# Optimization experiments

Measured on AMD Instinct MI355X. Metric: run time of the kernel, lower is better.

## Reference

```python
import jax, jax.numpy as jnp
import numpy as np

N_HEADS = 32
N_KV_HEADS = 8
HEAD_DIM = 128
ROPE_BASE = 10000.0
NEG_INF = -1e9


def rope(x, base=ROPE_BASE, offset=0):
    # x: [B, H, L, d]; 'traditional' RoPE with the module's rotation formula.
    d = x.shape[-1]
    t = jnp.arange(x.shape[2], dtype=jnp.float32) + offset
    freqs = base ** (-jnp.arange(0, d, 2, dtype=jnp.float32) / d)  # [d/2]
    ang = t[:, None] * freqs[None, :]                              # [L, d/2]
    cos, sin = jnp.cos(ang), jnp.sin(ang)
    x1, x2 = x[..., 0::2], x[..., 1::2]
    out = jnp.stack([x1 * cos + x2 * sin, x1 * sin - x2 * cos], axis=-1)
    return out.reshape(x.shape)


def setup_inputs() -> dict:
    key = jax.random.key(0)
    ks = jax.random.split(key, 5)
    B, L, D = 2, 2048, 4096
    x = jax.random.normal(ks[0], (B, L, D), dtype=jnp.float32)
    wq = jax.random.normal(ks[1], (D, N_HEADS * HEAD_DIM), dtype=jnp.float32) * 0.02
    wk = jax.random.normal(ks[2], (D, N_KV_HEADS * HEAD_DIM), dtype=jnp.float32) * 0.02
    wv = jax.random.normal(ks[3], (D, N_KV_HEADS * HEAD_DIM), dtype=jnp.float32) * 0.02
    wo = jax.random.normal(ks[4], (N_HEADS * HEAD_DIM, D), dtype=jnp.float32) * 0.02
    # causal additive mask [L, L]
    mask = jnp.where(jnp.tril(jnp.ones((L, L), dtype=bool)), 0.0, NEG_INF).astype(jnp.float32)
    return {"x": x, "mask": mask, "wq": wq, "wk": wk, "wv": wv, "wo": wo}


def reference(x, mask, wq, wk, wv, wo):
    B, L, D = x.shape
    scale = HEAD_DIM ** -0.5
    q = (x @ wq).reshape(B, L, N_HEADS, HEAD_DIM).transpose(0, 2, 1, 3)     # [B,H,L,d]
    k = (x @ wk).reshape(B, L, N_KV_HEADS, HEAD_DIM).transpose(0, 2, 1, 3)  # [B,Hk,L,d]
    v = (x @ wv).reshape(B, L, N_KV_HEADS, HEAD_DIM).transpose(0, 2, 1, 3)
    rep = N_HEADS // N_KV_HEADS
    k = jnp.repeat(k, rep, axis=1)  # [B,H,L,d]  (physical GQA repeat, as in source)
    v = jnp.repeat(v, rep, axis=1)
    q = rope(q)
    k = rope(k)
    scores = jnp.einsum("bhqd,bhkd->bhqk", q * scale, k) + mask  # [B,H,L,L]
    probs = jax.nn.softmax(scores.astype(jnp.float32), axis=-1).astype(scores.dtype)
    out = jnp.einsum("bhqk,bhkd->bhqd", probs, v)
    out = out.transpose(0, 2, 1, 3).reshape(B, L, N_HEADS * HEAD_DIM)
    return out @ wo, (k, v)
```

## Files before the change

kernel.cpp:

```cpp
#include <hip/hip_runtime.h>

typedef unsigned short u16;
typedef unsigned int u32;
typedef float f32x4 __attribute__((ext_vector_type(4)));
typedef u32 u32x2 __attribute__((ext_vector_type(2)));
typedef __bf16 bf16x8 __attribute__((ext_vector_type(8)));

#define DEV __device__ __forceinline__

DEV u16 f2b(float f) {
    union { float f; u32 u; } v; v.f = f;
    u32 r = v.u + 0x7fffu + ((v.u >> 16) & 1u);
    return (u16)(r >> 16);
}
DEV float b2f(u16 b) {
    union { u32 u; float f; } v; v.u = ((u32)b) << 16;
    return v.f;
}

DEV void gload16(const void* g, void* l) {
    __builtin_amdgcn_global_load_lds((const __attribute__((address_space(1))) void*)g,
                                     (__attribute__((address_space(3))) void*)l, 16, 0, 0);
}

DEV f32x4 mfma16(bf16x8 a, bf16x8 b, f32x4 c) {
    return __builtin_amdgcn_mfma_f32_16x16x32_bf16(a, b, c, 0, 0, 0);
}

__global__ __launch_bounds__(256) void convx_kernel(const float* __restrict__ in,
                                                    u16* __restrict__ out) {
    size_t i = ((size_t)blockIdx.x * 256 + threadIdx.x) * 4;
    float4 v = *(const float4*)(in + i);
    ushort4 o; o.x = f2b(v.x); o.y = f2b(v.y); o.z = f2b(v.z); o.w = f2b(v.w);
    *(ushort4*)(out + i) = o;
}

__global__ __launch_bounds__(256) void tconv_kernel(const float* __restrict__ in,
                                                    u16* __restrict__ out, int K, int N) {
    __shared__ float tile[64][65];
    int t = threadIdx.x;
    int n0 = blockIdx.x * 64, k0 = blockIdx.y * 64;
    int r = t >> 4, c4 = (t & 15) * 4;
#pragma unroll
    for (int i = 0; i < 4; ++i) {
        float4 v = *(const float4*)(in + (size_t)(k0 + i * 16 + r) * N + n0 + c4);
        tile[i * 16 + r][c4 + 0] = v.x; tile[i * 16 + r][c4 + 1] = v.y;
        tile[i * 16 + r][c4 + 2] = v.z; tile[i * 16 + r][c4 + 3] = v.w;
    }
    __syncthreads();
#pragma unroll
    for (int i = 0; i < 4; ++i) {
        int nn = i * 16 + r;
        ushort4 o;
        o.x = f2b(tile[c4 + 0][nn]); o.y = f2b(tile[c4 + 1][nn]);
        o.z = f2b(tile[c4 + 2][nn]); o.w = f2b(tile[c4 + 3][nn]);
        *(ushort4*)(out + (size_t)(n0 + nn) * K + k0 + c4) = o;
    }
}

#define GEMM128_BODY                                                                        \
    __shared__ __align__(16) u16 Asb[2][2][64 * 64];                                        \
    __shared__ __align__(16) u16 Bsb[2][2][64 * 64];                                        \
    int t = threadIdx.x;                                                                    \
    int lane = t & 63, w = t >> 6;                                                          \
    int wrM = w >> 1, wcN = w & 1;                                                          \
    int lr = lane & 15, hi = lane >> 4;                                                     \
    int wg = blockIdx.x;                                                                    \
    int swz = (wg & 7) * ((int)gridDim.x >> 3) + (wg >> 3);                                 \
    int bx = swz / gy, by = swz % gy;                                                       \
    int m0 = by * 128, n0 = bx * 128;                                                       \
    int nk = K >> 6;                                                                        \
    auto stageA = [&](int X, int h) {                                                       \
        const u16* src = A + (size_t)(m0 + h * 64) * K + X * 64;                            \
        char* dst = (char*)&Asb[X & 1][h][0];                                               \
        _Pragma("unroll")                                                                   \
        for (int it = 0; it < 2; ++it) {                                                    \
            int c = it * 256 + t;                                                           \
            int row = c >> 3;                                                               \
            int col8 = ((c & 7) ^ (row & 7)) << 3;                                          \
            gload16(src + (size_t)row * K + col8, dst + (it * 256 + (t & ~63)) * 16);       \
        }                                                                                   \
    };                                                                                      \
    auto stageB = [&](int X, int h) {                                                       \
        const u16* src = Bt + (size_t)(n0 + h * 64) * K + X * 64;                           \
        char* dst = (char*)&Bsb[X & 1][h][0];                                               \
        _Pragma("unroll")                                                                   \
        for (int it = 0; it < 2; ++it) {                                                    \
            int c = it * 256 + t;                                                           \
            int row = c >> 3;                                                               \
            int col8 = ((c & 7) ^ (row & 7)) << 3;                                          \
            gload16(src + (size_t)row * K + col8, dst + (it * 256 + (t & ~63)) * 16);       \
        }                                                                                   \
    };                                                                                      \
    stageA(0, 0); stageA(0, 1); stageB(0, 0); stageB(0, 1);                                 \
    stageA(1, 0); stageA(1, 1);                                                             \
    asm volatile("s_waitcnt vmcnt(4)" ::: "memory");                                        \
    __builtin_amdgcn_s_barrier();                                                           \
    f32x4 acc[4][4] = {};                                                                   \
    for (int kt = 0; kt < nk; ++kt) {                                                       \
        __builtin_amdgcn_sched_barrier(0);                                                  \
        int p = kt & 1;                                                                     \
        const char* Ah = (const char*)&Asb[p][wrM][0];                                      \
        const char* Bh = (const char*)&Bsb[p][wcN][0];                                      \
        bool s1 = (kt + 1 < nk), s2 = (kt + 2 < nk);                                        \
        bf16x8 a[4][2], bb[2][2];                                                           \
        _Pragma("unroll")                                                                   \
        for (int mf = 0; mf < 4; ++mf)                                                      \
            _Pragma("unroll")                                                               \
            for (int ks = 0; ks < 2; ++ks) {                                                \
                int row = mf * 16 + lr;                                                     \
                a[mf][ks] = *(const bf16x8*)(Ah + ((row * 128 + ks * 64 + hi * 16) ^ ((row & 7) << 4))); \
            }                                                                               \
        _Pragma("unroll")                                                                   \
        for (int nf = 0; nf < 2; ++nf)                                                      \
            _Pragma("unroll")                                                               \
            for (int ks = 0; ks < 2; ++ks) {                                                \
                int row = nf * 16 + lr;                                                     \
                bb[nf][ks] = *(const bf16x8*)(Bh + ((row * 128 + ks * 64 + hi * 16) ^ ((row & 7) << 4))); \
            }                                                                               \
        if (s1) { stageB(kt + 1, 0); stageB(kt + 1, 1); }                                   \
        __builtin_amdgcn_s_barrier();                                                       \
        __builtin_amdgcn_s_setprio(1);                                                      \
        _Pragma("unroll")                                                                   \
        for (int mf = 0; mf < 4; ++mf)                                                      \
            _Pragma("unroll")                                                               \
            for (int nf = 0; nf < 2; ++nf)                                                  \
                _Pragma("unroll")                                                           \
                for (int ks = 0; ks < 2; ++ks)                                              \
                    acc[mf][nf] = mfma16(a[mf][ks], bb[nf][ks], acc[mf][nf]);               \
        __builtin_amdgcn_s_setprio(0);                                                      \
        __builtin_amdgcn_s_barrier();                                                       \
        _Pragma("unroll")                                                                   \
        for (int nf = 0; nf < 2; ++nf)                                                      \
            _Pragma("unroll")                                                               \
            for (int ks = 0; ks < 2; ++ks) {                                                \
                int row = (nf + 2) * 16 + lr;                                               \
                bb[nf][ks] = *(const bf16x8*)(Bh + ((row * 128 + ks * 64 + hi * 16) ^ ((row & 7) << 4))); \
            }                                                                               \
        if (s2) { stageA(kt + 2, 0); stageA(kt + 2, 1); }                                   \
        __builtin_amdgcn_s_barrier();                                                       \
        __builtin_amdgcn_s_setprio(1);                                                      \
        _Pragma("unroll")                                                                   \
        for (int mf = 0; mf < 4; ++mf)                                                      \
            _Pragma("unroll")                                                               \
            for (int nf = 0; nf < 2; ++nf)                                                  \
                _Pragma("unroll")                                                           \
                for (int ks = 0; ks < 2; ++ks)                                              \
                    acc[mf][nf + 2] = mfma16(a[mf][ks], bb[nf][ks], acc[mf][nf + 2]);       \
        __builtin_amdgcn_s_setprio(0);                                                      \
        if (s2)      asm volatile("s_waitcnt vmcnt(4)" ::: "memory");                       \
        else if (s1) asm volatile("s_waitcnt vmcnt(0)" ::: "memory");                       \
        __builtin_amdgcn_s_barrier();                                                       \
    }

__global__ __launch_bounds__(256, 2) void gemm128_qkv_kernel(const u16* __restrict__ A,
                                                             const u16* __restrict__ Bt,
                                                             u16* __restrict__ Cb,
                                                             float* __restrict__ outk,
                                                             int N, int K, int gy) {
    GEMM128_BODY
    int isv = (n0 >= 5120);
    int isk = (n0 >= 4096) && !isv;
    int odd = lane & 1;
#pragma unroll
    for (int nf = 0; nf < 4; ++nf) {
        int n = n0 + wcN * 64 + nf * 16 + lr;
        int d = n & 127;
        float freq = exp2f((float)(d >> 1) * -0.2076205059304601f);
#pragma unroll
        for (int mf = 0; mf < 4; ++mf)
#pragma unroll
            for (int r = 0; r < 4; ++r) {
                int m = m0 + wrM * 64 + mf * 16 + hi * 4 + r;
                int l = m & 2047, bi = m >> 11;
                float val = acc[mf][nf][r];
                float pair = __shfl_xor(val, 1);
                float out = val;
                if (!isv) {
                    float sv, cv;
                    sincosf((float)l * freq, &sv, &cv);
                    out = odd ? (pair * sv - val * cv) : (val * cv + pair * sv);
                }
                Cb[(size_t)m * N + n] = f2b(out);
                if (isk) {
                    int kvh = (n - 4096) >> 7;
#pragma unroll
                    for (int rr = 0; rr < 4; ++rr)
                        outk[((size_t)((bi * 32 + kvh * 4 + rr) * 2048) + l) * 128 + d] = out;
                }
            }
    }
}

__global__ __launch_bounds__(256, 2) void gemm128_kernel(const u16* __restrict__ A,
                                                         const u16* __restrict__ Bt,
                                                         float* __restrict__ Cf,
                                                         int N, int K, int gy) {
    GEMM128_BODY
#pragma unroll
    for (int mf = 0; mf < 4; ++mf)
#pragma unroll
        for (int nf = 0; nf < 4; ++nf)
#pragma unroll
            for (int r = 0; r < 4; ++r) {
                int m = m0 + wrM * 64 + mf * 16 + hi * 4 + r;
                int n = n0 + wcN * 64 + nf * 16 + lr;
                Cf[(size_t)m * N + n] = acc[mf][nf][r];
            }
}

__global__ __launch_bounds__(256) void vtrans_kernel(const u16* __restrict__ qkv,
                                                     u16* __restrict__ vt,
                                                     float* __restrict__ outv) {
    __shared__ u16 tile[64][65];
    int t = threadIdx.x;
    int l0 = blockIdx.x * 64, d0 = blockIdx.y * 64;
    int z = blockIdx.z, b = z >> 3, kvh = z & 7;
    int r = t >> 4, c4 = (t & 15) * 4;
#pragma unroll
    for (int i = 0; i < 4; ++i) {
        int l = l0 + i * 16 + r;
        ushort4 v = *(const ushort4*)(qkv + (size_t)(b * 2048 + l) * 6144 + 5120 + kvh * 128 + d0 + c4);
        tile[i * 16 + r][c4 + 0] = v.x; tile[i * 16 + r][c4 + 1] = v.y;
        tile[i * 16 + r][c4 + 2] = v.z; tile[i * 16 + r][c4 + 3] = v.w;
        float4 f; f.x = b2f(v.x); f.y = b2f(v.y); f.z = b2f(v.z); f.w = b2f(v.w);
#pragma unroll
        for (int rr = 0; rr < 4; ++rr)
            *(float4*)(outv + ((size_t)((b * 32 + kvh * 4 + rr) * 2048) + l) * 128 + d0 + c4) = f;
    }
    __syncthreads();
#pragma unroll
    for (int i = 0; i < 4; ++i) {
        int dn = i * 16 + r;
        ushort4 o;
        o.x = tile[c4 + 0][dn]; o.y = tile[c4 + 1][dn];
        o.z = tile[c4 + 2][dn]; o.w = tile[c4 + 3][dn];
        *(ushort4*)(vt + (size_t)((b * 8 + kvh) * 128 + d0 + dn) * 2048 + l0 + c4) = o;
    }
}

__global__ __launch_bounds__(256, 2) void attn_kernel(const u16* __restrict__ qkv,
                                                      const u16* __restrict__ vt,
                                                      u16* __restrict__ ab) {
    __shared__ __align__(16) u16 Kbuf[2][64 * 128];
    __shared__ __align__(16) u16 Vbuf[2][128 * 64];
    __shared__ __align__(16) u16 Ps[4][32 * 64];
    int t = threadIdx.x, lane = t & 63, w = t >> 6;
    int lr = lane & 15, hi = lane >> 4;
    int h = blockIdx.y, b = blockIdx.z, kvh = h >> 2;

    const u16* kbase = qkv + (size_t)(b * 2048) * 6144 + 4096 + kvh * 128;
    const u16* vtbase = vt + (size_t)((b * 8 + kvh) * 128) * 2048;

    auto stageKV = [&](int k0, int buf) {
#pragma unroll
        for (int i = 0; i < 4; ++i) {
            int c = i * 256 + t;
            int row = c >> 4;
            int col8 = ((c & 15) ^ (row & 7)) << 3;
            gload16(kbase + (size_t)(k0 + row) * 6144 + col8,
                    (char*)Kbuf[buf] + (i * 256 + (t & ~63)) * 16);
        }
#pragma unroll
        for (int i = 0; i < 4; ++i) {
            int c = i * 256 + t;
            int row = c >> 3;
            int col8 = ((c & 7) ^ (row & 7)) << 3;
            gload16(vtbase + (size_t)row * 2048 + k0 + col8,
                    (char*)Vbuf[buf] + (i * 256 + (t & ~63)) * 16);
        }
    };

    auto process = [&](int qblk) {
        int q0 = qblk * 128;
        bf16x8 qf[2][4];
#pragma unroll
        for (int half = 0; half < 2; ++half)
#pragma unroll
            for (int kki = 0; kki < 4; ++kki)
                qf[half][kki] = *(const bf16x8*)(qkv +
                    (size_t)(b * 2048 + q0 + w * 32 + half * 16 + lr) * 6144 + h * 128 +
                    kki * 32 + 8 * hi);
        f32x4 acc[2][8] = {};
        float mrun[2] = {-1e30f, -1e30f}, lrun[2] = {0.f, 0.f};

        int nt = 2 * (qblk + 1);
        stageKV(0, 0);
        __syncthreads();
        int cur = 0;
        for (int kt = 0; kt < nt; ++kt) {
            if (kt + 1 < nt) stageKV((kt + 1) * 64, cur ^ 1);
            __builtin_amdgcn_sched_barrier(0);

            const u16* Ks = Kbuf[cur];
            const u16* Vs = Vbuf[cur];
            f32x4 s[2][4] = {};
            __builtin_amdgcn_s_setprio(1);
#pragma unroll
            for (int kki = 0; kki < 4; ++kki) {
                bf16x8 kf[4];
#pragma unroll
                for (int fc = 0; fc < 4; ++fc) {
                    int kvr = fc * 16 + lr;
                    int byt = (kvr * 256 + (kki * 32 + 8 * hi) * 2) ^ ((kvr & 7) << 4);
                    kf[fc] = *(const bf16x8*)((const char*)Ks + byt);
                }
#pragma unroll
                for (int fc = 0; fc < 4; ++fc) {
                    s[0][fc] = mfma16(kf[fc], qf[0][kki], s[0][fc]);
                    s[1][fc] = mfma16(kf[fc], qf[1][kki], s[1][fc]);
                }
            }
            __builtin_amdgcn_s_setprio(0);
            const float SC = 0.08838834764831845f;
            int domask = (kt >= nt - 2);
            u16* Pw = Ps[w];
#pragma unroll
            for (int half = 0; half < 2; ++half) {
                int qabs = q0 + w * 32 + half * 16 + lr;
#pragma unroll
                for (int fc = 0; fc < 4; ++fc)
#pragma unroll
                    for (int r = 0; r < 4; ++r) {
                        float v = s[half][fc][r] * SC;
                        if (domask && (kt * 64 + fc * 16 + hi * 4 + r) > qabs) v = -1e30f;
                        s[half][fc][r] = v;
                    }
                float pm = s[half][0][0];
#pragma unroll
                for (int fc = 0; fc < 4; ++fc)
#pragma unroll
                    for (int r = 0; r < 4; ++r) pm = fmaxf(pm, s[half][fc][r]);
                pm = fmaxf(pm, __shfl_xor(pm, 16));
                pm = fmaxf(pm, __shfl_xor(pm, 32));
                float mn = fmaxf(mrun[half], pm);
                float fr = __expf(mrun[half] - mn);
                mrun[half] = mn;
                float ls = 0.f;
#pragma unroll
                for (int fc = 0; fc < 4; ++fc)
#pragma unroll
                    for (int r = 0; r < 4; ++r) {
                        float e = __expf(s[half][fc][r] - mn);
                        s[half][fc][r] = e;
                        ls += e;
                    }
                ls += __shfl_xor(ls, 16);
                ls += __shfl_xor(ls, 32);
                lrun[half] = lrun[half] * fr + ls;
#pragma unroll
                for (int dhf = 0; dhf < 8; ++dhf)
#pragma unroll
                    for (int r = 0; r < 4; ++r) acc[half][dhf][r] *= fr;
#pragma unroll
                for (int fc = 0; fc < 4; ++fc) {
                    u32x2 pk;
                    pk.x = (u32)f2b(s[half][fc][0]) | ((u32)f2b(s[half][fc][1]) << 16);
                    pk.y = (u32)f2b(s[half][fc][2]) | ((u32)f2b(s[half][fc][3]) << 16);
                    int byt = (half * 2048 + lr * 128 + fc * 32 + hi * 8) ^ ((lr & 7) << 4);
                    *(u32x2*)((char*)Pw + byt) = pk;
                }
            }
            asm volatile("s_waitcnt lgkmcnt(0)" ::: "memory");
            __builtin_amdgcn_s_setprio(1);
#pragma unroll
            for (int kk2 = 0; kk2 < 2; ++kk2) {
                bf16x8 pf0 = *(const bf16x8*)((const char*)Pw +
                    ((lr * 128 + kk2 * 64 + hi * 16) ^ ((lr & 7) << 4)));
                bf16x8 pf1 = *(const bf16x8*)((const char*)Pw +
                    ((2048 + lr * 128 + kk2 * 64 + hi * 16) ^ ((lr & 7) << 4)));
#pragma unroll
                for (int dhf = 0; dhf < 8; ++dhf) {
                    int dh = dhf * 16 + lr;
                    int bytv = (dh * 128 + (kk2 * 32 + 8 * hi) * 2) ^ ((dh & 7) << 4);
                    bf16x8 vf = *(const bf16x8*)((const char*)Vs + bytv);
                    acc[0][dhf] = mfma16(vf, pf0, acc[0][dhf]);
                    acc[1][dhf] = mfma16(vf, pf1, acc[1][dhf]);
                }
            }
            __builtin_amdgcn_s_setprio(0);
            __syncthreads();
            cur ^= 1;
        }
#pragma unroll
        for (int half = 0; half < 2; ++half) {
            float inv = 1.0f / lrun[half];
            int qrow = q0 + w * 32 + half * 16 + lr;
#pragma unroll
            for (int dhf = 0; dhf < 8; ++dhf) {
                ushort4 o;
                o.x = f2b(acc[half][dhf][0] * inv); o.y = f2b(acc[half][dhf][1] * inv);
                o.z = f2b(acc[half][dhf][2] * inv); o.w = f2b(acc[half][dhf][3] * inv);
                *(ushort4*)(ab + (size_t)(b * 2048 + qrow) * 4096 + h * 128 + dhf * 16 + hi * 4) = o;
            }
        }
    };

    process(15 - blockIdx.x);
    __syncthreads();
    process(blockIdx.x);
}

extern "C" void kernel_launch(void* const* d_in, const int* in_sizes, int n_in,
                              void* d_out, int out_size, void* d_ws, size_t ws_size,
                              hipStream_t stream) {
    (void)in_sizes; (void)n_in; (void)out_size; (void)ws_size;
    const float* x  = (const float*)d_in[0];
    const float* wq = (const float*)d_in[2];
    const float* wk = (const float*)d_in[3];
    const float* wv = (const float*)d_in[4];
    const float* wo = (const float*)d_in[5];

    char* ws = (char*)d_ws;
    u16* xb  = (u16*)(ws + 0);
    u16* fBt = (u16*)(ws + 33554432);
    u16* qkv = (u16*)(ws + 83886080);
    u16* vt  = (u16*)(ws + 134217728);
    u16* ab  = xb;
    u16* wob = fBt;

    float* out0 = (float*)d_out;
    float* outk = out0 + 16777216;
    float* outv = out0 + 33554432;

    convx_kernel<<<16384, 256, 0, stream>>>(x, xb);
    tconv_kernel<<<dim3(64, 64), 256, 0, stream>>>(wq, fBt, 4096, 4096);
    tconv_kernel<<<dim3(16, 64), 256, 0, stream>>>(wk, fBt + (size_t)4096 * 4096, 4096, 1024);
    tconv_kernel<<<dim3(16, 64), 256, 0, stream>>>(wv, fBt + (size_t)5120 * 4096, 4096, 1024);

    gemm128_qkv_kernel<<<1536, 256, 0, stream>>>(xb, fBt, qkv, outk, 6144, 4096, 32);

    tconv_kernel<<<dim3(64, 64), 256, 0, stream>>>(wo, wob, 4096, 4096);

    vtrans_kernel<<<dim3(32, 2, 16), 256, 0, stream>>>(qkv, vt, outv);

    attn_kernel<<<dim3(8, 32, 2), 256, 0, stream>>>(qkv, vt, ab);

    gemm128_kernel<<<1024, 256, 0, stream>>>(ab, wob, out0, 4096, 4096, 32);
}
```

Measured before the change: 606.2 us.

## Replace QKV GEMM with K32 triple-buffered kernel and separate RoPE pass

Merges the three weight-transpose launches into one kernel. Swaps the fused QKV GEMM+RoPE epilogue for a new GEMM with 32-wide K steps, triple buffering and 3 blocks per CU, which writes plain bf16. RoPE and the repeated-K output move to a separate elementwise kernel. This removes the sincos and shuffle work from the GEMM epilogue and should raise occupancy, at the cost of an extra read/write pass over Q and K.

```diff
diff --git a/kernel.cpp b/kernel.cpp
--- a/kernel.cpp
+++ b/kernel.cpp
@@ -35,6 +35,35 @@
     *(ushort4*)(out + i) = o;
 }
 
+__global__ __launch_bounds__(256) void tconv3_kernel(const float* __restrict__ wq,
+                                                     const float* __restrict__ wk,
+                                                     const float* __restrict__ wv,
+                                                     u16* __restrict__ out) {
+    __shared__ float tile[64][65];
+    int t = threadIdx.x;
+    int n0 = blockIdx.x * 64, k0 = blockIdx.y * 64;
+    const float* src; int Ns, nl;
+    if (n0 < 4096)      { src = wq; Ns = 4096; nl = n0; }
+    else if (n0 < 5120) { src = wk; Ns = 1024; nl = n0 - 4096; }
+    else                { src = wv; Ns = 1024; nl = n0 - 5120; }
+    int r = t >> 4, c4 = (t & 15) * 4;
+#pragma unroll
+    for (int i = 0; i < 4; ++i) {
+        float4 v = *(const float4*)(src + (size_t)(k0 + i * 16 + r) * Ns + nl + c4);
+        tile[i * 16 + r][c4 + 0] = v.x; tile[i * 16 + r][c4 + 1] = v.y;
+        tile[i * 16 + r][c4 + 2] = v.z; tile[i * 16 + r][c4 + 3] = v.w;
+    }
+    __syncthreads();
+#pragma unroll
+    for (int i = 0; i < 4; ++i) {
+        int nn = i * 16 + r;
+        ushort4 o;
+        o.x = f2b(tile[c4 + 0][nn]); o.y = f2b(tile[c4 + 1][nn]);
+        o.z = f2b(tile[c4 + 2][nn]); o.w = f2b(tile[c4 + 3][nn]);
+        *(ushort4*)(out + (size_t)(n0 + nn) * 4096 + k0 + c4) = o;
+    }
+}
+
 __global__ __launch_bounds__(256) void tconv_kernel(const float* __restrict__ in,
                                                     u16* __restrict__ out, int K, int N) {
     __shared__ float tile[64][65];
@@ -56,6 +85,93 @@
         o.z = f2b(tile[c4 + 2][nn]); o.w = f2b(tile[c4 + 3][nn]);
         *(ushort4*)(out + (size_t)(n0 + nn) * K + k0 + c4) = o;
     }
+}
+
+__global__ __launch_bounds__(256, 3) void gemmk32_kernel(const u16* __restrict__ A,
+                                                         const u16* __restrict__ Bt,
+                                                         u16* __restrict__ Cb,
+                                                         int N, int K, int gy) {
+    __shared__ __align__(16) u16 Asb[3][128 * 32];
+    __shared__ __align__(16) u16 Bsb[3][128 * 32];
+    int t = threadIdx.x;
+    int lane = t & 63, w = t >> 6;
+    int wrM = w >> 1, wcN = w & 1;
+    int lr = lane & 15, hi = lane >> 4;
+    int wg = blockIdx.x;
+    int swz = (wg & 7) * ((int)gridDim.x >> 3) + (wg >> 3);
+    int bx = swz / gy, by = swz % gy;
+    int m0 = by * 128, n0 = bx * 128;
+    int nk = K >> 5;
+
+    auto stageA = [&](int X, int buf) {
+        const u16* src = A + (size_t)m0 * K + X * 32;
+        char* dst = (char*)&Asb[buf][0];
+#pragma unroll
+        for (int it = 0; it < 2; ++it) {
+            int c = it * 256 + t;
+            int row = c >> 2;
+            int col8 = ((c & 3) ^ ((row >> 1) & 3)) << 3;
+            gload16(src + (size_t)row * K + col8, dst + (it * 256 + (t & ~63)) * 16);
+        }
+    };
+    auto stageB = [&](int X, int buf) {
+        const u16* src = Bt + (size_t)n0 * K + X * 32;
+        char* dst = (char*)&Bsb[buf][0];
+#pragma unroll
+        for (int it = 0; it < 2; ++it) {
+            int c = it * 256 + t;
+            int row = c >> 2;
+            int col8 = ((c & 3) ^ ((row >> 1) & 3)) << 3;
+            gload16(src + (size_t)row * K + col8, dst + (it * 256 + (t & ~63)) * 16);
+        }
+    };
+
+    stageA(0, 0); stageB(0, 0); stageA(1, 1); stageB(1, 1);
+    asm volatile("s_waitcnt vmcnt(4)" ::: "memory");
+    __builtin_amdgcn_s_barrier();
+
+    f32x4 acc[4][4] = {};
+    for (int kt = 0; kt < nk; ++kt) {
+        __builtin_amdgcn_sched_barrier(0);
+        int p = kt % 3;
+        const char* Ah = (const char*)&Asb[p][0] + wrM * 4096;
+        const char* Bh = (const char*)&Bsb[p][0] + wcN * 4096;
+        bool s2 = (kt + 2 < nk), s1 = (kt + 1 < nk);
+        bf16x8 a[4], bb[4];
+#pragma unroll
+        for (int mf = 0; mf < 4; ++mf) {
+            int row = mf * 16 + lr;
+            a[mf] = *(const bf16x8*)(Ah + ((row * 64 + hi * 16) ^ (((row >> 1) & 3) << 4)));
+        }
+#pragma unroll
+        for (int nf = 0; nf < 4; ++nf) {
+            int row = nf * 16 + lr;
+            bb[nf] = *(const bf16x8*)(Bh + ((row * 64 + hi * 16) ^ (((row >> 1) & 3) << 4)));
+        }
+        if (s2) { int b2 = (kt + 2) % 3; stageA(kt + 2, b2); stageB(kt + 2, b2); }
+        __builtin_amdgcn_s_barrier();
+        __builtin_amdgcn_s_setprio(1);
+#pragma unroll
+        for (int mf = 0; mf < 4; ++mf)
+#pragma unroll
+            for (int nf = 0; nf < 4; ++nf)
+                acc[mf][nf] = mfma16(a[mf], bb[nf], acc[mf][nf]);
+        __builtin_amdgcn_s_setprio(0);
+        if (s2)      asm volatile("s_waitcnt vmcnt(4)" ::: "memory");
+        else if (s1) asm volatile("s_waitcnt vmcnt(0)" ::: "memory");
+        __builtin_amdgcn_s_barrier();
+    }
+
+#pragma unroll
+    for (int mf = 0; mf < 4; ++mf)
+#pragma unroll
+        for (int nf = 0; nf < 4; ++nf)
+#pragma unroll
+            for (int r = 0; r < 4; ++r) {
+                int m = m0 + wrM * 64 + mf * 16 + hi * 4 + r;
+                int n = n0 + wcN * 64 + nf * 16 + lr;
+                Cb[(size_t)m * N + n] = f2b(acc[mf][nf][r]);
+            }
 }
 
 #define GEMM128_BODY                                                                        \
@@ -153,45 +269,6 @@
         __builtin_amdgcn_s_barrier();                                                       \
     }
 
-__global__ __launch_bounds__(256, 2) void gemm128_qkv_kernel(const u16* __restrict__ A,
-                                                             const u16* __restrict__ Bt,
-                                                             u16* __restrict__ Cb,
-                                                             float* __restrict__ outk,
-                                                             int N, int K, int gy) {
-    GEMM128_BODY
-    int isv = (n0 >= 5120);
-    int isk = (n0 >= 4096) && !isv;
-    int odd = lane & 1;
-#pragma unroll
-    for (int nf = 0; nf < 4; ++nf) {
-        int n = n0 + wcN * 64 + nf * 16 + lr;
-        int d = n & 127;
-        float freq = exp2f((float)(d >> 1) * -0.2076205059304601f);
-#pragma unroll
-        for (int mf = 0; mf < 4; ++mf)
-#pragma unroll
-            for (int r = 0; r < 4; ++r) {
-                int m = m0 + wrM * 64 + mf * 16 + hi * 4 + r;
-                int l = m & 2047, bi = m >> 11;
-                float val = acc[mf][nf][r];
-                float pair = __shfl_xor(val, 1);
-                float out = val;
-                if (!isv) {
-                    float sv, cv;
-                    sincosf((float)l * freq, &sv, &cv);
-                    out = odd ? (pair * sv - val * cv) : (val * cv + pair * sv);
-                }
-                Cb[(size_t)m * N + n] = f2b(out);
-                if (isk) {
-                    int kvh = (n - 4096) >> 7;
-#pragma unroll
-                    for (int rr = 0; rr < 4; ++rr)
-                        outk[((size_t)((bi * 32 + kvh * 4 + rr) * 2048) + l) * 128 + d] = out;
-                }
-            }
-    }
-}
-
 __global__ __launch_bounds__(256, 2) void gemm128_kernel(const u16* __restrict__ A,
                                                          const u16* __restrict__ Bt,
                                                          float* __restrict__ Cf,
@@ -207,6 +284,35 @@
                 int n = n0 + wcN * 64 + nf * 16 + lr;
                 Cf[(size_t)m * N + n] = acc[mf][nf][r];
             }
+}
+
+__global__ __launch_bounds__(256) void rope_kernel(u16* __restrict__ qkv,
+                                                   float* __restrict__ outk) {
+    int row = blockIdx.y;
+    int p = blockIdx.x * 256 + threadIdx.x;
+    int b = row >> 11, l = row & 2047;
+    float freq = exp2f((float)(p & 63) * -0.2076205059304601f);
+    float sv, cv; sincosf((float)l * freq, &sv, &cv);
+    if (p < 2048) {
+        int h = p >> 6, i = p & 63;
+        size_t idx = (size_t)row * 6144 + h * 128 + 2 * i;
+        u32 pr = *(const u32*)(qkv + idx);
+        float x1 = b2f((u16)(pr & 0xffff)), x2 = b2f((u16)(pr >> 16));
+        float o1 = x1 * cv + x2 * sv, o2 = x1 * sv - x2 * cv;
+        *(u32*)(qkv + idx) = (u32)f2b(o1) | ((u32)f2b(o2) << 16);
+    } else {
+        int kvh = (p >> 6) - 32, i = p & 63;
+        size_t idx = (size_t)row * 6144 + 4096 + kvh * 128 + 2 * i;
+        u32 pr = *(const u32*)(qkv + idx);
+        float x1 = b2f((u16)(pr & 0xffff)), x2 = b2f((u16)(pr >> 16));
+        float o1 = x1 * cv + x2 * sv, o2 = x1 * sv - x2 * cv;
+        *(u32*)(qkv + idx) = (u32)f2b(o1) | ((u32)f2b(o2) << 16);
+#pragma unroll
+        for (int r = 0; r < 4; ++r) {
+            float2 o; o.x = o1; o.y = o2;
+            *(float2*)(outk + ((size_t)((b * 32 + kvh * 4 + r) * 2048) + l) * 128 + 2 * i) = o;
+        }
+    }
 }
 
 __global__ __launch_bounds__(256) void vtrans_kernel(const u16* __restrict__ qkv,
@@ -424,14 +530,13 @@
     float* outv = out0 + 33554432;
 
     convx_kernel<<<16384, 256, 0, stream>>>(x, xb);
-    tconv_kernel<<<dim3(64, 64), 256, 0, stream>>>(wq, fBt, 4096, 4096);
-    tconv_kernel<<<dim3(16, 64), 256, 0, stream>>>(wk, fBt + (size_t)4096 * 4096, 4096, 1024);
-    tconv_kernel<<<dim3(16, 64), 256, 0, stream>>>(wv, fBt + (size_t)5120 * 4096, 4096, 1024);
-
-    gemm128_qkv_kernel<<<1536, 256, 0, stream>>>(xb, fBt, qkv, outk, 6144, 4096, 32);
+    tconv3_kernel<<<dim3(96, 64), 256, 0, stream>>>(wq, wk, wv, fBt);
+
+    gemmk32_kernel<<<1536, 256, 0, stream>>>(xb, fBt, qkv, 6144, 4096, 32);
 
     tconv_kernel<<<dim3(64, 64), 256, 0, stream>>>(wo, wob, 4096, 4096);
 
+    rope_kernel<<<dim3(10, 4096), 256, 0, stream>>>(qkv, outk);
     vtrans_kernel<<<dim3(32, 2, 16), 256, 0, stream>>>(qkv, vt, outv);
 
     attn_kernel<<<dim3(8, 32, 2), 256, 0, stream>>>(qkv, vt, ab);
```

Result: slower. 621.8 us (+2.6%).

## Move RoPE and K export out of QKV GEMM epilogue into fused postprocess kernel

Applied to the files above, without the earlier changes.

The RoPE rotation and the fp32 K-cache writes are removed from the QKV GEMM epilogue. A new combined postprocess kernel rotates Q/K in place on the bf16 qkv buffer, writes the repeated fp32 K output, and also performs the V transpose and V export. The three weight transpose-convert launches are merged into one kernel. The aim is to lighten the GEMM epilogue, where sincos work and scattered fp32 stores hurt, at the cost of an extra read-modify-write pass over Q/K and an added bf16 round trip before rotation.

```diff
diff --git a/kernel.cpp b/kernel.cpp
--- a/kernel.cpp
+++ b/kernel.cpp
@@ -33,6 +33,35 @@
     float4 v = *(const float4*)(in + i);
     ushort4 o; o.x = f2b(v.x); o.y = f2b(v.y); o.z = f2b(v.z); o.w = f2b(v.w);
     *(ushort4*)(out + i) = o;
+}
+
+__global__ __launch_bounds__(256) void tconv3_kernel(const float* __restrict__ wq,
+                                                     const float* __restrict__ wk,
+                                                     const float* __restrict__ wv,
+                                                     u16* __restrict__ out) {
+    __shared__ float tile[64][65];
+    int t = threadIdx.x;
+    int n0 = blockIdx.x * 64, k0 = blockIdx.y * 64;
+    const float* src; int Ns, nl;
+    if (n0 < 4096)      { src = wq; Ns = 4096; nl = n0; }
+    else if (n0 < 5120) { src = wk; Ns = 1024; nl = n0 - 4096; }
+    else                { src = wv; Ns = 1024; nl = n0 - 5120; }
+    int r = t >> 4, c4 = (t & 15) * 4;
+#pragma unroll
+    for (int i = 0; i < 4; ++i) {
+        float4 v = *(const float4*)(src + (size_t)(k0 + i * 16 + r) * Ns + nl + c4);
+        tile[i * 16 + r][c4 + 0] = v.x; tile[i * 16 + r][c4 + 1] = v.y;
+        tile[i * 16 + r][c4 + 2] = v.z; tile[i * 16 + r][c4 + 3] = v.w;
+    }
+    __syncthreads();
+#pragma unroll
+    for (int i = 0; i < 4; ++i) {
+        int nn = i * 16 + r;
+        ushort4 o;
+        o.x = f2b(tile[c4 + 0][nn]); o.y = f2b(tile[c4 + 1][nn]);
+        o.z = f2b(tile[c4 + 2][nn]); o.w = f2b(tile[c4 + 3][nn]);
+        *(ushort4*)(out + (size_t)(n0 + nn) * 4096 + k0 + c4) = o;
+    }
 }
 
 __global__ __launch_bounds__(256) void tconv_kernel(const float* __restrict__ in,
@@ -153,49 +182,27 @@
         __builtin_amdgcn_s_barrier();                                                       \
     }
 
-__global__ __launch_bounds__(256, 2) void gemm128_qkv_kernel(const u16* __restrict__ A,
-                                                             const u16* __restrict__ Bt,
-                                                             u16* __restrict__ Cb,
-                                                             float* __restrict__ outk,
-                                                             int N, int K, int gy) {
+__global__ __launch_bounds__(256, 2) void gemm128_bf16_kernel(const u16* __restrict__ A,
+                                                              const u16* __restrict__ Bt,
+                                                              u16* __restrict__ Cb,
+                                                              int N, int K, int gy) {
     GEMM128_BODY
-    int isv = (n0 >= 5120);
-    int isk = (n0 >= 4096) && !isv;
-    int odd = lane & 1;
-#pragma unroll
-    for (int nf = 0; nf < 4; ++nf) {
-        int n = n0 + wcN * 64 + nf * 16 + lr;
-        int d = n & 127;
-        float freq = exp2f((float)(d >> 1) * -0.2076205059304601f);
-#pragma unroll
-        for (int mf = 0; mf < 4; ++mf)
+#pragma unroll
+    for (int mf = 0; mf < 4; ++mf)
+#pragma unroll
+        for (int nf = 0; nf < 4; ++nf)
 #pragma unroll
             for (int r = 0; r < 4; ++r) {
                 int m = m0 + wrM * 64 + mf * 16 + hi * 4 + r;
-                int l = m & 2047, bi = m >> 11;
-                float val = acc[mf][nf][r];
-                float pair = __shfl_xor(val, 1);
-                float out = val;
-                if (!isv) {
-                    float sv, cv;
-                    sincosf((float)l * freq, &sv, &cv);
-                    out = odd ? (pair * sv - val * cv) : (val * cv + pair * sv);
-                }
-                Cb[(size_t)m * N + n] = f2b(out);
-                if (isk) {
-                    int kvh = (n - 4096) >> 7;
-#pragma unroll
-                    for (int rr = 0; rr < 4; ++rr)
-                        outk[((size_t)((bi * 32 + kvh * 4 + rr) * 2048) + l) * 128 + d] = out;
-                }
-            }
-    }
-}
-
-__global__ __launch_bounds__(256, 2) void gemm128_kernel(const u16* __restrict__ A,
-                                                         const u16* __restrict__ Bt,
-                                                         float* __restrict__ Cf,
-                                                         int N, int K, int gy) {
+                int n = n0 + wcN * 64 + nf * 16 + lr;
+                Cb[(size_t)m * N + n] = f2b(acc[mf][nf][r]);
+            }
+}
+
+__global__ __launch_bounds__(256, 2) void gemm128_f32_kernel(const u16* __restrict__ A,
+                                                             const u16* __restrict__ Bt,
+                                                             float* __restrict__ Cf,
+                                                             int N, int K, int gy) {
     GEMM128_BODY
 #pragma unroll
     for (int mf = 0; mf < 4; ++mf)
@@ -209,33 +216,64 @@
             }
 }
 
-__global__ __launch_bounds__(256) void vtrans_kernel(const u16* __restrict__ qkv,
-                                                     u16* __restrict__ vt,
-                                                     float* __restrict__ outv) {
-    __shared__ u16 tile[64][65];
-    int t = threadIdx.x;
-    int l0 = blockIdx.x * 64, d0 = blockIdx.y * 64;
-    int z = blockIdx.z, b = z >> 3, kvh = z & 7;
-    int r = t >> 4, c4 = (t & 15) * 4;
-#pragma unroll
-    for (int i = 0; i < 4; ++i) {
-        int l = l0 + i * 16 + r;
-        ushort4 v = *(const ushort4*)(qkv + (size_t)(b * 2048 + l) * 6144 + 5120 + kvh * 128 + d0 + c4);
-        tile[i * 16 + r][c4 + 0] = v.x; tile[i * 16 + r][c4 + 1] = v.y;
-        tile[i * 16 + r][c4 + 2] = v.z; tile[i * 16 + r][c4 + 3] = v.w;
-        float4 f; f.x = b2f(v.x); f.y = b2f(v.y); f.z = b2f(v.z); f.w = b2f(v.w);
-#pragma unroll
-        for (int rr = 0; rr < 4; ++rr)
-            *(float4*)(outv + ((size_t)((b * 32 + kvh * 4 + rr) * 2048) + l) * 128 + d0 + c4) = f;
-    }
-    __syncthreads();
-#pragma unroll
-    for (int i = 0; i < 4; ++i) {
-        int dn = i * 16 + r;
-        ushort4 o;
-        o.x = tile[c4 + 0][dn]; o.y = tile[c4 + 1][dn];
-        o.z = tile[c4 + 2][dn]; o.w = tile[c4 + 3][dn];
-        *(ushort4*)(vt + (size_t)((b * 8 + kvh) * 128 + d0 + dn) * 2048 + l0 + c4) = o;
+__global__ __launch_bounds__(256) void postproc_kernel(u16* __restrict__ qkv,
+                                                       float* __restrict__ outk,
+                                                       u16* __restrict__ vt,
+                                                       float* __restrict__ outv) {
+    int id = blockIdx.x;
+    int tid = threadIdx.x;
+    if (id < 40960) {
+        int row = id / 10;
+        int p = (id % 10) * 256 + tid;
+        int b = row >> 11, l = row & 2047;
+        float freq = exp2f((float)(p & 63) * -0.2076205059304601f);
+        float sv, cv; sincosf((float)l * freq, &sv, &cv);
+        if (p < 2048) {
+            int h = p >> 6, i = p & 63;
+            size_t idx = (size_t)row * 6144 + h * 128 + 2 * i;
+            u32 pr = *(const u32*)(qkv + idx);
+            float x1 = b2f((u16)(pr & 0xffff)), x2 = b2f((u16)(pr >> 16));
+            float o1 = x1 * cv + x2 * sv, o2 = x1 * sv - x2 * cv;
+            *(u32*)(qkv + idx) = (u32)f2b(o1) | ((u32)f2b(o2) << 16);
+        } else {
+            int kvh = (p >> 6) - 32, i = p & 63;
+            size_t idx = (size_t)row * 6144 + 4096 + kvh * 128 + 2 * i;
+            u32 pr = *(const u32*)(qkv + idx);
+            float x1 = b2f((u16)(pr & 0xffff)), x2 = b2f((u16)(pr >> 16));
+            float o1 = x1 * cv + x2 * sv, o2 = x1 * sv - x2 * cv;
+            *(u32*)(qkv + idx) = (u32)f2b(o1) | ((u32)f2b(o2) << 16);
+#pragma unroll
+            for (int r = 0; r < 4; ++r) {
+                float2 o; o.x = o1; o.y = o2;
+                *(float2*)(outk + ((size_t)((b * 32 + kvh * 4 + r) * 2048) + l) * 128 + 2 * i) = o;
+            }
+        }
+    } else {
+        __shared__ u16 tile[64][65];
+        int i0 = id - 40960;
+        int l0 = (i0 & 31) * 64, d0 = ((i0 >> 5) & 1) * 64;
+        int z = i0 >> 6, b = z >> 3, kvh = z & 7;
+        int r = tid >> 4, c4 = (tid & 15) * 4;
+#pragma unroll
+        for (int i = 0; i < 4; ++i) {
+            int l = l0 + i * 16 + r;
+            ushort4 v = *(const ushort4*)(qkv + (size_t)(b * 2048 + l) * 6144 + 5120 + kvh * 128 + d0 + c4);
+            tile[i * 16 + r][c4 + 0] = v.x; tile[i * 16 + r][c4 + 1] = v.y;
+            tile[i * 16 + r][c4 + 2] = v.z; tile[i * 16 + r][c4 + 3] = v.w;
+            float4 f; f.x = b2f(v.x); f.y = b2f(v.y); f.z = b2f(v.z); f.w = b2f(v.w);
+#pragma unroll
+            for (int rr = 0; rr < 4; ++rr)
+                *(float4*)(outv + ((size_t)((b * 32 + kvh * 4 + rr) * 2048) + l) * 128 + d0 + c4) = f;
+        }
+        __syncthreads();
+#pragma unroll
+        for (int i = 0; i < 4; ++i) {
+            int dn = i * 16 + r;
+            ushort4 o;
+            o.x = tile[c4 + 0][dn]; o.y = tile[c4 + 1][dn];
+            o.z = tile[c4 + 2][dn]; o.w = tile[c4 + 3][dn];
+            *(ushort4*)(vt + (size_t)((b * 8 + kvh) * 128 + d0 + dn) * 2048 + l0 + c4) = o;
+        }
     }
 }
 
@@ -424,17 +462,15 @@
     float* outv = out0 + 33554432;
 
     convx_kernel<<<16384, 256, 0, stream>>>(x, xb);
-    tconv_kernel<<<dim3(64, 64), 256, 0, stream>>>(wq, fBt, 4096, 4096);
-    tconv_kernel<<<dim3(16, 64), 256, 0, stream>>>(wk, fBt + (size_t)4096 * 4096, 4096, 1024);
-    tconv_kernel<<<dim3(16, 64), 256, 0, stream>>>(wv, fBt + (size_t)5120 * 4096, 4096, 1024);
-
-    gemm128_qkv_kernel<<<1536, 256, 0, stream>>>(xb, fBt, qkv, outk, 6144, 4096, 32);
+    tconv3_kernel<<<dim3(96, 64), 256, 0, stream>>>(wq, wk, wv, fBt);
+
+    gemm128_bf16_kernel<<<1536, 256, 0, stream>>>(xb, fBt, qkv, 6144, 4096, 32);
 
     tconv_kernel<<<dim3(64, 64), 256, 0, stream>>>(wo, wob, 4096, 4096);
 
-    vtrans_kernel<<<dim3(32, 2, 16), 256, 0, stream>>>(qkv, vt, outv);
+    postproc_kernel<<<41984, 256, 0, stream>>>(qkv, outk, vt, outv);
 
     attn_kernel<<<dim3(8, 32, 2), 256, 0, stream>>>(qkv, vt, ab);
 
-    gemm128_kernel<<<1024, 256, 0, stream>>>(ab, wob, out0, 4096, 4096, 32);
-}
+    gemm128_f32_kernel<<<1024, 256, 0, stream>>>(ab, wob, out0, 4096, 4096, 32);
+}
```

After: 580.9 us, median of 2. 4.2% less time.
